# Kernel optimization log

Measured on AMD Instinct MI355X. Metric: run time of the kernel, lower is better.

Reference implementation:

```python
import jax, jax.numpy as jnp
import numpy as np

D_MODEL = 128
NUM_HEADS = 8
HEAD_DIM = D_MODEL // NUM_HEADS
LN_EPS = 1e-5


def layernorm(x, gamma, beta):
    mu = jnp.mean(x, axis=-1, keepdims=True)
    var = jnp.mean(jnp.square(x - mu), axis=-1, keepdims=True)
    return (x - mu) * jax.lax.rsqrt(var + LN_EPS) * gamma + beta


def setup_inputs() -> dict:
    key = jax.random.key(0)
    ks = jax.random.split(key, 12)
    B, L, d = 16, 1024, D_MODEL
    scale = 1.0 / np.sqrt(d)
    edge_x = jax.random.normal(ks[0], (B, L, d), dtype=jnp.float32)
    # True entries are masked out (masked_fill with -inf)
    edge_mask = jax.random.randint(ks[1], (B, L, L), 0, 2).astype(jnp.bool_)
    in_proj_w = jax.random.normal(ks[2], (d, 3 * d), dtype=jnp.float32) * scale  # fused QKV
    in_proj_b = jnp.zeros((3 * d,), dtype=jnp.float32)
    w1 = jax.random.normal(ks[3], (d, d), dtype=jnp.float32) * scale
    b1 = jnp.zeros((d,), dtype=jnp.float32)
    w2 = jax.random.normal(ks[4], (d, d), dtype=jnp.float32) * scale
    b2 = jnp.zeros((d,), dtype=jnp.float32)
    g1 = jnp.ones((d,), dtype=jnp.float32)
    beta1 = jnp.zeros((d,), dtype=jnp.float32)
    g2 = jnp.ones((d,), dtype=jnp.float32)
    beta2 = jnp.zeros((d,), dtype=jnp.float32)
    return {"edge_x": edge_x, "edge_mask": edge_mask, "in_proj_w": in_proj_w,
            "in_proj_b": in_proj_b, "w1": w1, "b1": b1, "w2": w2, "b2": b2,
            "g1": g1, "beta1": beta1, "g2": g2, "beta2": beta2}


def reference(edge_x, edge_mask, in_proj_w, in_proj_b, w1, b1, w2, b2, g1, beta1, g2, beta2):
    B, L, d = edge_x.shape
    H, hd = NUM_HEADS, HEAD_DIM
    scaling = float(hd) ** -0.5
    # fused QKV projection
    qkv = edge_x @ in_proj_w + in_proj_b              # [B, L, 3d]
    q, k, v = jnp.split(qkv, 3, axis=-1)
    q = q.reshape(B, L, H, hd).transpose(0, 2, 1, 3)  # [B, H, L, hd]
    k = k.reshape(B, L, H, hd).transpose(0, 2, 1, 3)
    v = v.reshape(B, L, H, hd).transpose(0, 2, 1, 3)
    scores = jnp.einsum('bhqd,bhkd->bhqk', q, k) * scaling  # [B, H, L, L]
    scores = jnp.where(edge_mask[:, None, :, :], -jnp.inf, scores)
    attn = jax.nn.softmax(scores, axis=-1)
    ctx = jnp.einsum('bhqk,bhkd->bhqd', attn, v)      # [B, H, L, hd]
    ctx = ctx.transpose(0, 2, 1, 3).reshape(B, L, d)
    # residual + LayerNorm
    x = layernorm(edge_x + ctx, g1, beta1)
    # FFN (relu), residual + LayerNorm (dropout=0 in eval mode)
    ff = jax.nn.relu(x @ w1 + b1) @ w2 + b2
    x = layernorm(x + ff, g2, beta2)
    return x
```

## Files before the change

kernel.cpp:

```cpp
#include <hip/hip_runtime.h>
#include <cstdint>

#define NROWS 16384
#define ARRE ((size_t)NROWS * 128)

typedef short short8 __attribute__((ext_vector_type(8)));
typedef float f32x4  __attribute__((ext_vector_type(4)));
typedef float f32x16 __attribute__((ext_vector_type(16)));

static __device__ __forceinline__ unsigned short f2bf(float f) {
    union { float f; uint32_t u; } v; v.f = f;
    uint32_t r = v.u + 0x7fffu + ((v.u >> 16) & 1u);
    return (unsigned short)(r >> 16);
}

static __device__ __forceinline__ uint32_t cvt_pk_bf16(float lo, float hi) {
    uint32_t r;
    asm("v_cvt_pk_bf16_f32 %0, %1, %2" : "=v"(r) : "v"(lo), "v"(hi));
    return r;
}

static __device__ __forceinline__ float v_exp2(float x) {
    float r;
    asm("v_exp_f32 %0, %1" : "=v"(r) : "v"(x));
    return r;
}

__global__ void k_castw(const float* __restrict__ wqkv, const float* __restrict__ w1,
                        const float* __restrict__ w2, unsigned short* __restrict__ wT,
                        const uint32_t* __restrict__ mask, int* __restrict__ flag)
{
    if (blockIdx.x == 320) {
        if (threadIdx.x == 0) {
            int f = 0;
            for (int i = 0; i < 256; ++i) f |= (mask[i] > 1u) ? 1 : 0;
            *flag = f;
        }
        return;
    }
    const int e = blockIdx.x * 256 + threadIdx.x;
    if (e < 49152) {
        const int n = e >> 7, k = e & 127;
        wT[e] = f2bf(wqkv[k * 384 + n]);
    } else if (e < 65536) {
        const int i = e - 49152, n = i >> 7, k = i & 127;
        wT[e] = f2bf(w1[k * 128 + n]);
    } else if (e < 81920) {
        const int i = e - 65536, n = i >> 7, k = i & 127;
        wT[e] = f2bf(w2[k * 128 + n]);
    }
}

template<int NF, int MODE>
__global__ __launch_bounds__(256, 2) void k_mm(const float* __restrict__ Xf,
        const unsigned short* __restrict__ Wt, const float* __restrict__ bias,
        unsigned short* __restrict__ out)
{
    __shared__ char smem[16384 + NF * 4096];
    char* const sX = smem;
    char* const sW = smem + 16384;
    const int t = threadIdx.x;
    const int w = t >> 6, l = t & 63;
    const int l4 = l >> 4, l15 = l & 15;
    const int r0 = blockIdx.x * 64;
    const int c0 = blockIdx.y * (NF * 16);

    #pragma unroll
    for (int i = 0; i < 4; ++i) {
        const int c = t + 256 * i;
        const int row = c >> 4, slot = c & 15;
        const float4* src = (const float4*)(Xf + (size_t)(r0 + row) * 128 + slot * 8);
        float4 f0 = src[0], f1 = src[1];
        uint4 v;
        v.x = cvt_pk_bf16(f0.x, f0.y);
        v.y = cvt_pk_bf16(f0.z, f0.w);
        v.z = cvt_pk_bf16(f1.x, f1.y);
        v.w = cvt_pk_bf16(f1.z, f1.w);
        *(uint4*)(sX + row * 256 + ((slot ^ (row & 15)) << 4)) = v;
    }
    #pragma unroll
    for (int i = 0; i < NF; ++i) {
        const int c = t + 256 * i;
        const int col = c >> 4, slot = c & 15;
        uint4 v = *(const uint4*)(Wt + (size_t)(c0 + col) * 128 + slot * 8);
        *(uint4*)(sW + col * 256 + ((slot ^ (col & 15)) << 4)) = v;
    }
    __syncthreads();

    short8 aF[4];
    #pragma unroll
    for (int kk = 0; kk < 4; ++kk)
        aF[kk] = *(const short8*)(sX + (w * 16 + l15) * 256 + (((kk * 4 + l4) ^ l15) << 4));

    f32x4 acc[NF];
    #pragma unroll
    for (int nf = 0; nf < NF; ++nf) acc[nf] = f32x4{0.f, 0.f, 0.f, 0.f};
    #pragma unroll
    for (int nf = 0; nf < NF; ++nf) {
        #pragma unroll
        for (int kk = 0; kk < 4; ++kk) {
            short8 bF = *(const short8*)(sW + (nf * 16 + l15) * 256 + (((kk * 4 + l4) ^ l15) << 4));
            acc[nf] = __builtin_amdgcn_mfma_f32_16x16x32_bf16(bF, aF[kk], acc[nf], 0, 0, 0);
        }
    }

    const float scl = (MODE == 0 && blockIdx.y == 0) ? 0.36067376022224085f : 1.0f;
    const int row = r0 + w * 16 + l15;
    #pragma unroll
    for (int nf = 0; nf < NF; ++nf) {
        const int cb = nf * 16 + l4 * 4;
        float4 bv = *(const float4*)(bias + c0 + cb);
        float v0 = acc[nf][0] + bv.x, v1 = acc[nf][1] + bv.y;
        float v2 = acc[nf][2] + bv.z, v3 = acc[nf][3] + bv.w;
        if (MODE == 1) {
            v0 = fmaxf(v0, 0.f); v1 = fmaxf(v1, 0.f);
            v2 = fmaxf(v2, 0.f); v3 = fmaxf(v3, 0.f);
        }
        v0 *= scl; v1 *= scl; v2 *= scl; v3 *= scl;
        uint2 pk;
        pk.x = cvt_pk_bf16(v0, v1);
        pk.y = cvt_pk_bf16(v2, v3);
        size_t o;
        if (MODE == 0) o = (size_t)blockIdx.y * ARRE + (size_t)row * 128 + cb;
        else           o = (size_t)row * 128 + c0 + cb;
        *(uint2*)(out + o) = pk;
    }
}

__global__ __launch_bounds__(256, 2) void k_ffn(const float* __restrict__ x1,
        const unsigned short* __restrict__ w1t, const float* __restrict__ b1,
        const unsigned short* __restrict__ w2t, const float* __restrict__ b2,
        const float* __restrict__ g2, const float* __restrict__ be2,
        float* __restrict__ out)
{
    __shared__ char smem[49152];
    char* const sX = smem;
    char* const sW = smem + 16384;
    const int t = threadIdx.x;
    const int w = t >> 6, l = t & 63;
    const int l4 = l >> 4, l15 = l & 15;
    const int r0 = blockIdx.x * 64;

    #pragma unroll
    for (int i = 0; i < 4; ++i) {
        const int c = t + 256 * i;
        const int row = c >> 4, slot = c & 15;
        const float4* src = (const float4*)(x1 + (size_t)(r0 + row) * 128 + slot * 8);
        float4 f0 = src[0], f1 = src[1];
        uint4 v;
        v.x = cvt_pk_bf16(f0.x, f0.y);
        v.y = cvt_pk_bf16(f0.z, f0.w);
        v.z = cvt_pk_bf16(f1.x, f1.y);
        v.w = cvt_pk_bf16(f1.z, f1.w);
        *(uint4*)(sX + row * 256 + ((slot ^ (row & 15)) << 4)) = v;
    }
    #pragma unroll
    for (int i = 0; i < 8; ++i) {
        const int c = t + 256 * i;
        const int col = c >> 4, slot = c & 15;
        uint4 v = *(const uint4*)(w1t + (size_t)col * 128 + slot * 8);
        *(uint4*)(sW + col * 256 + ((slot ^ (col & 15)) << 4)) = v;
    }
    __syncthreads();

    short8 aF[4];
    #pragma unroll
    for (int kk = 0; kk < 4; ++kk)
        aF[kk] = *(const short8*)(sX + (w * 16 + l15) * 256 + (((kk * 4 + l4) ^ l15) << 4));

    f32x4 acc[8];
    #pragma unroll
    for (int nf = 0; nf < 8; ++nf) acc[nf] = f32x4{0.f, 0.f, 0.f, 0.f};
    #pragma unroll
    for (int nf = 0; nf < 8; ++nf) {
        #pragma unroll
        for (int kk = 0; kk < 4; ++kk) {
            short8 bF = *(const short8*)(sW + (nf * 16 + l15) * 256 + (((kk * 4 + l4) ^ l15) << 4));
            acc[nf] = __builtin_amdgcn_mfma_f32_16x16x32_bf16(bF, aF[kk], acc[nf], 0, 0, 0);
        }
    }
    __syncthreads();

    {
        const int hrow = w * 16 + l15;
        #pragma unroll
        for (int nf = 0; nf < 8; ++nf) {
            const int cb = nf * 16 + l4 * 4;
            float4 bv = *(const float4*)(b1 + cb);
            float v0 = fmaxf(acc[nf][0] + bv.x, 0.f);
            float v1 = fmaxf(acc[nf][1] + bv.y, 0.f);
            float v2 = fmaxf(acc[nf][2] + bv.z, 0.f);
            float v3 = fmaxf(acc[nf][3] + bv.w, 0.f);
            uint2 pk;
            pk.x = cvt_pk_bf16(v0, v1);
            pk.y = cvt_pk_bf16(v2, v3);
            const int slot = (2 * nf) + (l4 >> 1);
            const int off  = (l4 & 1) * 8;
            *(uint2*)(sX + hrow * 256 + ((slot ^ (hrow & 15)) << 4) + off) = pk;
        }
    }
    #pragma unroll
    for (int i = 0; i < 8; ++i) {
        const int c = t + 256 * i;
        const int col = c >> 4, slot = c & 15;
        uint4 v = *(const uint4*)(w2t + (size_t)col * 128 + slot * 8);
        *(uint4*)(sW + col * 256 + ((slot ^ (col & 15)) << 4)) = v;
    }
    __syncthreads();

    short8 aG[4];
    #pragma unroll
    for (int kk = 0; kk < 4; ++kk)
        aG[kk] = *(const short8*)(sX + (w * 16 + l15) * 256 + (((kk * 4 + l4) ^ l15) << 4));

    f32x4 acc2[8];
    #pragma unroll
    for (int nf = 0; nf < 8; ++nf) acc2[nf] = f32x4{0.f, 0.f, 0.f, 0.f};
    #pragma unroll
    for (int nf = 0; nf < 8; ++nf) {
        #pragma unroll
        for (int kk = 0; kk < 4; ++kk) {
            short8 bF = *(const short8*)(sW + (nf * 16 + l15) * 256 + (((kk * 4 + l4) ^ l15) << 4));
            acc2[nf] = __builtin_amdgcn_mfma_f32_16x16x32_bf16(bF, aG[kk], acc2[nf], 0, 0, 0);
        }
    }

    const int row = r0 + w * 16 + l15;
    float y[8][4];
    float s = 0.f;
    #pragma unroll
    for (int nf = 0; nf < 8; ++nf) {
        const int cb = nf * 16 + l4 * 4;
        float4 bv = *(const float4*)(b2 + cb);
        float4 xv = *(const float4*)(x1 + (size_t)row * 128 + cb);
        y[nf][0] = acc2[nf][0] + bv.x + xv.x;
        y[nf][1] = acc2[nf][1] + bv.y + xv.y;
        y[nf][2] = acc2[nf][2] + bv.z + xv.z;
        y[nf][3] = acc2[nf][3] + bv.w + xv.w;
        s += y[nf][0] + y[nf][1] + y[nf][2] + y[nf][3];
    }
    s += __shfl_xor(s, 16); s += __shfl_xor(s, 32);
    const float mu = s * (1.f / 128.f);
    float vv = 0.f;
    #pragma unroll
    for (int nf = 0; nf < 8; ++nf) {
        #pragma unroll
        for (int reg = 0; reg < 4; ++reg) { float d = y[nf][reg] - mu; vv += d * d; }
    }
    vv += __shfl_xor(vv, 16); vv += __shfl_xor(vv, 32);
    const float rs = rsqrtf(vv * (1.f / 128.f) + 1e-5f);
    #pragma unroll
    for (int nf = 0; nf < 8; ++nf) {
        const int cb = nf * 16 + l4 * 4;
        float4 gv = *(const float4*)(g2 + cb);
        float4 ev = *(const float4*)(be2 + cb);
        float4 o;
        o.x = (y[nf][0] - mu) * rs * gv.x + ev.x;
        o.y = (y[nf][1] - mu) * rs * gv.y + ev.y;
        o.z = (y[nf][2] - mu) * rs * gv.z + ev.z;
        o.w = (y[nf][3] - mu) * rs * gv.w + ev.w;
        *(float4*)(out + (size_t)row * 128 + cb) = o;
    }
}

__global__ __launch_bounds__(512, 2) void k_attn(
        const unsigned short* __restrict__ qb,
        const unsigned short* __restrict__ kb,
        const unsigned short* __restrict__ vbp,
        const void* __restrict__ maskp, const int* __restrict__ flag,
        const float* __restrict__ x, const float* __restrict__ g1,
        const float* __restrict__ be1, float* __restrict__ x1)
{
    __shared__ alignas(16) char smem[41216];
    char*          const sK  = smem;
    char*          const sVT = smem + 9216;
    char*          const sP  = smem + 19584;
    unsigned char* const sM  = (unsigned char*)(smem + 40064);
    float*         const sS  = (float*)(smem + 40192);

    const int t  = threadIdx.x;
    const int w  = t >> 6;
    const int l  = t & 63;
    const int bid = blockIdx.x;
    const int b  = ((bid & 7) << 1) | ((bid >> 3) >> 5);
    const int q0 = ((bid >> 3) & 31) * 32;
    const int q   = l & 31;
    const int hi  = l >> 5;
    const int l4  = l >> 4;
    const int l15 = l & 15;
    const int bytemask = *flag;

    short8 qf;
    {
        const size_t qrow = (size_t)(b * 1024 + q0 + q) * 128;
        qf = *(const short8*)(qb + qrow + w * 16 + hi * 8);
    }
    float m = -INFINITY, ls = 0.f;
    f32x4 ac0 = {0,0,0,0}, ac1 = {0,0,0,0};
    const f32x16 z16 = {};
    float* const sSw = sS + w * 32;
    char*  const Pw  = sP + w * 2560;

    const uint8_t* m8  = (const uint8_t*)maskp;
    const int*     m32 = (const int*)maskp;

    for (int kt = 0; kt < 32; ++kt) {
        const int k0 = kt * 32;
        __syncthreads();
        {
            const int row = t >> 4, slot = t & 15;
            const size_t src = (size_t)(b * 1024 + k0 + row) * 128 + slot * 8;
            uint4 kv = *(const uint4*)(kb + src);
            *(uint4*)(sK + row * 288 + ((slot ^ (row & 15)) << 4)) = kv;
            uint4 vv = *(const uint4*)(vbp + src);
            char* vt = sVT + (slot >> 1) * 1296 + (slot & 1) * 640 + row * 2;
            const uint32_t w0 = vv.x, w1 = vv.y, w2 = vv.z, w3 = vv.w;
            *(unsigned short*)(vt + 0 * 80) = (unsigned short)(w0);
            *(unsigned short*)(vt + 1 * 80) = (unsigned short)(w0 >> 16);
            *(unsigned short*)(vt + 2 * 80) = (unsigned short)(w1);
            *(unsigned short*)(vt + 3 * 80) = (unsigned short)(w1 >> 16);
            *(unsigned short*)(vt + 4 * 80) = (unsigned short)(w2);
            *(unsigned short*)(vt + 5 * 80) = (unsigned short)(w2 >> 16);
            *(unsigned short*)(vt + 6 * 80) = (unsigned short)(w3);
            *(unsigned short*)(vt + 7 * 80) = (unsigned short)(w3 >> 16);
        }
        if (t < 128) {
            const int mq = t >> 2, g = t & 3;
            const size_t moff = ((size_t)b << 20) + (size_t)(q0 + mq) * 1024
                              + (size_t)(k0 + g * 8);
            unsigned int bits = 0;
            if (bytemask) {
                uint64_t v = *(const uint64_t*)(m8 + moff);
                #pragma unroll
                for (int j = 0; j < 8; ++j)
                    bits |= ((((v >> (8 * j)) & 0xffull) == 0ull) ? 1u : 0u) << j;
            } else {
                const int4* p = (const int4*)(m32 + moff);
                int4 va = p[0], vc = p[1];
                bits = (va.x==0?1u:0u) | (va.y==0?2u:0u) | (va.z==0?4u:0u) | (va.w==0?8u:0u)
                     | (vc.x==0?16u:0u) | (vc.y==0?32u:0u) | (vc.z==0?64u:0u) | (vc.w==0?128u:0u);
            }
            sM[mq * 4 + g] = (unsigned char)bits;
        }
        __syncthreads();

        const uint32_t mk = *(const uint32_t*)(sM + q * 4);
        const uint32_t mks = mk >> (4 * hi);

        short8 kf = *(const short8*)(sK + q * 288 + ((((w << 1) + hi) ^ (q & 15)) << 4));
        f32x16 sc = __builtin_amdgcn_mfma_f32_32x32x16_bf16(kf, qf, z16, 0, 0, 0);
        float sm = sc[0];
        #pragma unroll
        for (int r = 1; r < 16; ++r) sm = fmaxf(sm, sc[r]);
        sm = fmaxf(sm, __shfl_xor(sm, 32));
        if (__any(sm > m + 8.f)) {
            float nm = fmaxf(m, sm);
            float s  = v_exp2(m - nm);
            m = nm; ls *= s;
            sSw[q] = s;
            float4 s0v = *(float4*)&sSw[l4 * 4];
            float4 s1v = *(float4*)&sSw[l4 * 4 + 16];
            ac0[0] *= s0v.x; ac0[1] *= s0v.y; ac0[2] *= s0v.z; ac0[3] *= s0v.w;
            ac1[0] *= s1v.x; ac1[1] *= s1v.y; ac1[2] *= s1v.z; ac1[3] *= s1v.w;
        }
        float p[16]; float lsum = 0.f;
        #pragma unroll
        for (int r = 0; r < 16; ++r) {
            const int c = (r & 3) + 8 * (r >> 2);
            float pv = v_exp2(sc[r] - m);
            pv = ((mks >> c) & 1u) ? pv : 0.f;
            lsum += pv; p[r] = pv;
        }
        ls += lsum;
        #pragma unroll
        for (int g = 0; g < 4; ++g) {
            uint2 pk;
            pk.x = cvt_pk_bf16(p[4*g+0], p[4*g+1]);
            pk.y = cvt_pk_bf16(p[4*g+2], p[4*g+3]);
            *(uint2*)(Pw + q * 80 + (8 * g + 4 * hi) * 2) = pk;
        }
        short8 pa0 = *(const short8*)(Pw + l15 * 80 + l4 * 16);
        short8 pa1 = *(const short8*)(Pw + (l15 + 16) * 80 + l4 * 16);
        short8 vf  = *(const short8*)(sVT + w * 1296 + l15 * 80 + l4 * 16);
        ac0 = __builtin_amdgcn_mfma_f32_16x16x32_bf16(pa0, vf, ac0, 0, 0, 0);
        ac1 = __builtin_amdgcn_mfma_f32_16x16x32_bf16(pa1, vf, ac1, 0, 0, 0);
    }

    __syncthreads();
    float* const sC = (float*)smem;
    {
        float lt  = ls + __shfl_xor(ls, 32);
        float inv = 1.f / lt;
        sSw[q] = inv;
        float4 i0 = *(float4*)&sSw[l4 * 4];
        float4 i1 = *(float4*)&sSw[l4 * 4 + 16];
        const int cc = w * 16 + l15;
        sC[(l4 * 4 + 0) * 132 + cc]  = ac0[0] * i0.x;
        sC[(l4 * 4 + 1) * 132 + cc]  = ac0[1] * i0.y;
        sC[(l4 * 4 + 2) * 132 + cc]  = ac0[2] * i0.z;
        sC[(l4 * 4 + 3) * 132 + cc]  = ac0[3] * i0.w;
        sC[(l4 * 4 + 16) * 132 + cc] = ac1[0] * i1.x;
        sC[(l4 * 4 + 17) * 132 + cc] = ac1[1] * i1.y;
        sC[(l4 * 4 + 18) * 132 + cc] = ac1[2] * i1.z;
        sC[(l4 * 4 + 19) * 132 + cc] = ac1[3] * i1.w;
    }
    __syncthreads();

    {
        const int row = t >> 4;
        const int c0  = (t & 15) * 8;
        const size_t grow = (size_t)(b * 1024 + q0 + row);
        const float4* xp = (const float4*)(x + grow * 128 + c0);
        const float4* cp = (const float4*)(sC + row * 132 + c0);
        float y[8];
        float s = 0.f;
        #pragma unroll
        for (int j = 0; j < 2; ++j) {
            float4 xv = xp[j], cv = cp[j];
            y[4*j+0] = xv.x + cv.x; y[4*j+1] = xv.y + cv.y;
            y[4*j+2] = xv.z + cv.z; y[4*j+3] = xv.w + cv.w;
            s += y[4*j+0] + y[4*j+1] + y[4*j+2] + y[4*j+3];
        }
        s += __shfl_xor(s, 1); s += __shfl_xor(s, 2);
        s += __shfl_xor(s, 4); s += __shfl_xor(s, 8);
        const float mu = s * (1.f / 128.f);
        float vv = 0.f;
        #pragma unroll
        for (int e = 0; e < 8; ++e) { float d = y[e] - mu; vv += d * d; }
        vv += __shfl_xor(vv, 1); vv += __shfl_xor(vv, 2);
        vv += __shfl_xor(vv, 4); vv += __shfl_xor(vv, 8);
        const float rs = rsqrtf(vv * (1.f / 128.f) + 1e-5f);
        #pragma unroll
        for (int j = 0; j < 2; ++j) {
            float4 gv = *(const float4*)(g1 + c0 + 4 * j);
            float4 bv = *(const float4*)(be1 + c0 + 4 * j);
            float4 o;
            o.x = (y[4*j+0] - mu) * rs * gv.x + bv.x;
            o.y = (y[4*j+1] - mu) * rs * gv.y + bv.y;
            o.z = (y[4*j+2] - mu) * rs * gv.z + bv.z;
            o.w = (y[4*j+3] - mu) * rs * gv.w + bv.w;
            *(float4*)(x1 + grow * 128 + c0 + 4 * j) = o;
        }
    }
}

extern "C" void kernel_launch(void* const* d_in, const int* in_sizes, int n_in,
                              void* d_out, int out_size, void* d_ws, size_t ws_size,
                              hipStream_t stream)
{
    const float* x    = (const float*)d_in[0];
    const void*  mask = d_in[1];
    const float* wqkv = (const float*)d_in[2];
    const float* bqkv = (const float*)d_in[3];
    const float* w1   = (const float*)d_in[4];
    const float* b1   = (const float*)d_in[5];
    const float* w2   = (const float*)d_in[6];
    const float* b2   = (const float*)d_in[7];
    const float* g1   = (const float*)d_in[8];
    const float* be1  = (const float*)d_in[9];
    const float* g2   = (const float*)d_in[10];
    const float* be2  = (const float*)d_in[11];
    float* out = (float*)d_out;

    char* base = (char*)d_ws;
    int* flag = (int*)base;
    unsigned short* qb  = (unsigned short*)(base + 256);
    unsigned short* kb  = qb + ARRE;
    unsigned short* vb  = kb + ARRE;
    float* x1           = (float*)(base + 256 + (size_t)12 * 1024 * 1024);
    unsigned short* wT  = (unsigned short*)(base + 256 + (size_t)20 * 1024 * 1024);

    k_castw<<<321, 256, 0, stream>>>(wqkv, w1, w2, wT, (const uint32_t*)mask, flag);
    k_mm<8, 0><<<dim3(256, 3), 256, 0, stream>>>(x, wT, bqkv, qb);
    k_attn<<<512, 512, 0, stream>>>(qb, kb, vb, mask, flag, x, g1, be1, x1);
    k_ffn<<<256, 256, 0, stream>>>(x1, wT + 49152, b1, wT + 65536, b2, g2, be2, out);
}
```

Baseline: 197.5 us.

## Prefetch next K/V/mask tile into registers and keep P in registers for PV

The attention kernel now loads the next key tile's K, V and mask data into registers right after the barrier, so global loads overlap with compute instead of sitting in the critical path. The P·V product switches from two 16x16 MFMAs fed through an LDS staging buffer to two 32x32x16 MFMAs whose P operand is built with cross-half lane shuffles. This removes the sP and scale-broadcast LDS buffers and shrinks shared memory so launch bounds can request 4 blocks per CU. The trade-off is higher register pressure from the prefetch registers under a tighter register cap, and a redundant wraparound load on the last iteration.

```diff
diff --git a/kernel.cpp b/kernel.cpp
--- a/kernel.cpp
+++ b/kernel.cpp
@@ -263,7 +263,7 @@
     }
 }
 
-__global__ __launch_bounds__(512, 2) void k_attn(
+__global__ __launch_bounds__(512, 4) void k_attn(
         const unsigned short* __restrict__ qb,
         const unsigned short* __restrict__ kb,
         const unsigned short* __restrict__ vbp,
@@ -271,97 +271,112 @@
         const float* __restrict__ x, const float* __restrict__ g1,
         const float* __restrict__ be1, float* __restrict__ x1)
 {
-    __shared__ alignas(16) char smem[41216];
+    __shared__ alignas(16) char smem[18688];
     char*          const sK  = smem;
-    char*          const sVT = smem + 9216;
-    char*          const sP  = smem + 19584;
-    unsigned char* const sM  = (unsigned char*)(smem + 40064);
-    float*         const sS  = (float*)(smem + 40192);
+    char*          const sVT = smem + 8192;
+    unsigned char* const sM  = (unsigned char*)(smem + 18560);
 
     const int t  = threadIdx.x;
     const int w  = t >> 6;
     const int l  = t & 63;
     const int bid = blockIdx.x;
-    const int b  = ((bid & 7) << 1) | ((bid >> 3) >> 5);
+    const int b  = ((bid & 7) << 1) | (bid >> 8);
     const int q0 = ((bid >> 3) & 31) * 32;
-    const int q   = l & 31;
-    const int hi  = l >> 5;
-    const int l4  = l >> 4;
-    const int l15 = l & 15;
+    const int q  = l & 31;
+    const int hi = l >> 5;
     const int bytemask = *flag;
 
-    short8 qf;
-    {
-        const size_t qrow = (size_t)(b * 1024 + q0 + q) * 128;
-        qf = *(const short8*)(qb + qrow + w * 16 + hi * 8);
-    }
+    const short8 qf = *(const short8*)(qb + (size_t)(b * 1024 + q0 + q) * 128 + w * 16 + hi * 8);
+
+    const int srow = t >> 4, sslot = t & 15;
+    const size_t gbase = (size_t)(b * 1024 + srow) * 128 + sslot * 8;
+    char* const wK = sK + srow * 256 + ((sslot ^ (srow & 15)) << 4);
+    const int vh = sslot >> 1, vs = sslot & 1;
+    char* const wV = sVT + vh * 1296 + ((2 * srow + 16 * vs) & 63);
+    const int mq = t >> 2, mg = t & 3;
+    const size_t mbase = ((size_t)b << 20) + (size_t)(q0 + mq) * 1024 + mg * 8;
+
+    const char* const rK = sK + q * 256 + ((((w << 1) | hi) ^ (q & 15)) << 4);
+    const int dd = l & 15, sp = dd >> 3;
+    const char* const rV = sVT + w * 1296 + dd * 80;
+    const int vo0 = (16 * hi + 16 * sp) & 63;
+    const int vo1 = (32 + 16 * hi + 16 * sp) & 63;
+
+    uint4 kv, vv, ma = {0,0,0,0}, mb = {0,0,0,0};
+    kv = *(const uint4*)(kb + gbase);
+    vv = *(const uint4*)(vbp + gbase);
+    if (t < 128) {
+        if (bytemask) {
+            uint2 v = *(const uint2*)((const uint8_t*)maskp + mbase);
+            ma.x = v.x; ma.y = v.y;
+        } else {
+            const uint4* p4 = (const uint4*)((const int*)maskp + mbase);
+            ma = p4[0]; mb = p4[1];
+        }
+    }
+
     float m = -INFINITY, ls = 0.f;
-    f32x4 ac0 = {0,0,0,0}, ac1 = {0,0,0,0};
+    f32x16 acc = {};
     const f32x16 z16 = {};
-    float* const sSw = sS + w * 32;
-    char*  const Pw  = sP + w * 2560;
-
-    const uint8_t* m8  = (const uint8_t*)maskp;
-    const int*     m32 = (const int*)maskp;
+    union U8 { uint4 u; short8 s; };
 
     for (int kt = 0; kt < 32; ++kt) {
-        const int k0 = kt * 32;
         __syncthreads();
+        *(uint4*)wK = kv;
         {
-            const int row = t >> 4, slot = t & 15;
-            const size_t src = (size_t)(b * 1024 + k0 + row) * 128 + slot * 8;
-            uint4 kv = *(const uint4*)(kb + src);
-            *(uint4*)(sK + row * 288 + ((slot ^ (row & 15)) << 4)) = kv;
-            uint4 vv = *(const uint4*)(vbp + src);
-            char* vt = sVT + (slot >> 1) * 1296 + (slot & 1) * 640 + row * 2;
             const uint32_t w0 = vv.x, w1 = vv.y, w2 = vv.z, w3 = vv.w;
-            *(unsigned short*)(vt + 0 * 80) = (unsigned short)(w0);
-            *(unsigned short*)(vt + 1 * 80) = (unsigned short)(w0 >> 16);
-            *(unsigned short*)(vt + 2 * 80) = (unsigned short)(w1);
-            *(unsigned short*)(vt + 3 * 80) = (unsigned short)(w1 >> 16);
-            *(unsigned short*)(vt + 4 * 80) = (unsigned short)(w2);
-            *(unsigned short*)(vt + 5 * 80) = (unsigned short)(w2 >> 16);
-            *(unsigned short*)(vt + 6 * 80) = (unsigned short)(w3);
-            *(unsigned short*)(vt + 7 * 80) = (unsigned short)(w3 >> 16);
+            *(unsigned short*)(wV + (8 * vs + 0) * 80) = (unsigned short)(w0);
+            *(unsigned short*)(wV + (8 * vs + 1) * 80) = (unsigned short)(w0 >> 16);
+            *(unsigned short*)(wV + (8 * vs + 2) * 80) = (unsigned short)(w1);
+            *(unsigned short*)(wV + (8 * vs + 3) * 80) = (unsigned short)(w1 >> 16);
+            *(unsigned short*)(wV + (8 * vs + 4) * 80) = (unsigned short)(w2);
+            *(unsigned short*)(wV + (8 * vs + 5) * 80) = (unsigned short)(w2 >> 16);
+            *(unsigned short*)(wV + (8 * vs + 6) * 80) = (unsigned short)(w3);
+            *(unsigned short*)(wV + (8 * vs + 7) * 80) = (unsigned short)(w3 >> 16);
         }
         if (t < 128) {
-            const int mq = t >> 2, g = t & 3;
-            const size_t moff = ((size_t)b << 20) + (size_t)(q0 + mq) * 1024
-                              + (size_t)(k0 + g * 8);
             unsigned int bits = 0;
             if (bytemask) {
-                uint64_t v = *(const uint64_t*)(m8 + moff);
+                uint64_t v = (uint64_t)ma.x | ((uint64_t)ma.y << 32);
                 #pragma unroll
                 for (int j = 0; j < 8; ++j)
                     bits |= ((((v >> (8 * j)) & 0xffull) == 0ull) ? 1u : 0u) << j;
             } else {
-                const int4* p = (const int4*)(m32 + moff);
-                int4 va = p[0], vc = p[1];
-                bits = (va.x==0?1u:0u) | (va.y==0?2u:0u) | (va.z==0?4u:0u) | (va.w==0?8u:0u)
-                     | (vc.x==0?16u:0u) | (vc.y==0?32u:0u) | (vc.z==0?64u:0u) | (vc.w==0?128u:0u);
+                bits = (ma.x==0?1u:0u) | (ma.y==0?2u:0u) | (ma.z==0?4u:0u) | (ma.w==0?8u:0u)
+                     | (mb.x==0?16u:0u) | (mb.y==0?32u:0u) | (mb.z==0?64u:0u) | (mb.w==0?128u:0u);
             }
-            sM[mq * 4 + g] = (unsigned char)bits;
+            sM[mq * 4 + mg] = (unsigned char)bits;
         }
         __syncthreads();
-
-        const uint32_t mk = *(const uint32_t*)(sM + q * 4);
-        const uint32_t mks = mk >> (4 * hi);
-
-        short8 kf = *(const short8*)(sK + q * 288 + ((((w << 1) + hi) ^ (q & 15)) << 4));
+        {
+            const int kn = (kt + 1) & 31;
+            const size_t g = gbase + (size_t)kn * 4096;
+            kv = *(const uint4*)(kb + g);
+            vv = *(const uint4*)(vbp + g);
+            if (t < 128) {
+                const size_t mo = mbase + (size_t)kn * 32;
+                if (bytemask) {
+                    uint2 v = *(const uint2*)((const uint8_t*)maskp + mo);
+                    ma.x = v.x; ma.y = v.y;
+                } else {
+                    const uint4* p4 = (const uint4*)((const int*)maskp + mo);
+                    ma = p4[0]; mb = p4[1];
+                }
+            }
+        }
+        const uint32_t mks = (*(const uint32_t*)(sM + q * 4)) >> (4 * hi);
+        const short8 kf = *(const short8*)rK;
         f32x16 sc = __builtin_amdgcn_mfma_f32_32x32x16_bf16(kf, qf, z16, 0, 0, 0);
         float sm = sc[0];
         #pragma unroll
         for (int r = 1; r < 16; ++r) sm = fmaxf(sm, sc[r]);
         sm = fmaxf(sm, __shfl_xor(sm, 32));
         if (__any(sm > m + 8.f)) {
-            float nm = fmaxf(m, sm);
-            float s  = v_exp2(m - nm);
+            const float nm = fmaxf(m, sm);
+            const float s = v_exp2(m - nm);
             m = nm; ls *= s;
-            sSw[q] = s;
-            float4 s0v = *(float4*)&sSw[l4 * 4];
-            float4 s1v = *(float4*)&sSw[l4 * 4 + 16];
-            ac0[0] *= s0v.x; ac0[1] *= s0v.y; ac0[2] *= s0v.z; ac0[3] *= s0v.w;
-            ac1[0] *= s1v.x; ac1[1] *= s1v.y; ac1[2] *= s1v.z; ac1[3] *= s1v.w;
+            #pragma unroll
+            for (int r = 0; r < 8; ++r) acc[r] *= s;
         }
         float p[16]; float lsum = 0.f;
         #pragma unroll
@@ -372,37 +387,32 @@
             lsum += pv; p[r] = pv;
         }
         ls += lsum;
-        #pragma unroll
-        for (int g = 0; g < 4; ++g) {
-            uint2 pk;
-            pk.x = cvt_pk_bf16(p[4*g+0], p[4*g+1]);
-            pk.y = cvt_pk_bf16(p[4*g+2], p[4*g+3]);
-            *(uint2*)(Pw + q * 80 + (8 * g + 4 * hi) * 2) = pk;
-        }
-        short8 pa0 = *(const short8*)(Pw + l15 * 80 + l4 * 16);
-        short8 pa1 = *(const short8*)(Pw + (l15 + 16) * 80 + l4 * 16);
-        short8 vf  = *(const short8*)(sVT + w * 1296 + l15 * 80 + l4 * 16);
-        ac0 = __builtin_amdgcn_mfma_f32_16x16x32_bf16(pa0, vf, ac0, 0, 0, 0);
-        ac1 = __builtin_amdgcn_mfma_f32_16x16x32_bf16(pa1, vf, ac1, 0, 0, 0);
+        const uint32_t cA0 = cvt_pk_bf16(p[0],  p[1]),  cA1 = cvt_pk_bf16(p[2],  p[3]);
+        const uint32_t cB0 = cvt_pk_bf16(p[4],  p[5]),  cB1 = cvt_pk_bf16(p[6],  p[7]);
+        const uint32_t cC0 = cvt_pk_bf16(p[8],  p[9]),  cC1 = cvt_pk_bf16(p[10], p[11]);
+        const uint32_t cD0 = cvt_pk_bf16(p[12], p[13]), cD1 = cvt_pk_bf16(p[14], p[15]);
+        const uint32_t xA0 = __shfl_xor(cA0, 32), xA1 = __shfl_xor(cA1, 32);
+        const uint32_t xB0 = __shfl_xor(cB0, 32), xB1 = __shfl_xor(cB1, 32);
+        const uint32_t xC0 = __shfl_xor(cC0, 32), xC1 = __shfl_xor(cC1, 32);
+        const uint32_t xD0 = __shfl_xor(cD0, 32), xD1 = __shfl_xor(cD1, 32);
+        U8 pb0, pb1;
+        pb0.u = hi ? uint4{xB0, xB1, cB0, cB1} : uint4{cA0, cA1, xA0, xA1};
+        pb1.u = hi ? uint4{xD0, xD1, cD0, cD1} : uint4{cC0, cC1, xC0, xC1};
+        const short8 va0 = *(const short8*)(rV + vo0);
+        const short8 va1 = *(const short8*)(rV + vo1);
+        acc = __builtin_amdgcn_mfma_f32_32x32x16_bf16(va0, pb0.s, acc, 0, 0, 0);
+        acc = __builtin_amdgcn_mfma_f32_32x32x16_bf16(va1, pb1.s, acc, 0, 0, 0);
     }
 
     __syncthreads();
     float* const sC = (float*)smem;
     {
-        float lt  = ls + __shfl_xor(ls, 32);
-        float inv = 1.f / lt;
-        sSw[q] = inv;
-        float4 i0 = *(float4*)&sSw[l4 * 4];
-        float4 i1 = *(float4*)&sSw[l4 * 4 + 16];
-        const int cc = w * 16 + l15;
-        sC[(l4 * 4 + 0) * 132 + cc]  = ac0[0] * i0.x;
-        sC[(l4 * 4 + 1) * 132 + cc]  = ac0[1] * i0.y;
-        sC[(l4 * 4 + 2) * 132 + cc]  = ac0[2] * i0.z;
-        sC[(l4 * 4 + 3) * 132 + cc]  = ac0[3] * i0.w;
-        sC[(l4 * 4 + 16) * 132 + cc] = ac1[0] * i1.x;
-        sC[(l4 * 4 + 17) * 132 + cc] = ac1[1] * i1.y;
-        sC[(l4 * 4 + 18) * 132 + cc] = ac1[2] * i1.z;
-        sC[(l4 * 4 + 19) * 132 + cc] = ac1[3] * i1.w;
+        const float inv = 1.f / (ls + __shfl_xor(ls, 32));
+        float* const row = sC + q * 132 + w * 16 + 4 * hi;
+        row[0] = acc[0] * inv; row[1] = acc[1] * inv;
+        row[2] = acc[2] * inv; row[3] = acc[3] * inv;
+        row[8] = acc[4] * inv; row[9] = acc[5] * inv;
+        row[10] = acc[6] * inv; row[11] = acc[7] * inv;
     }
     __syncthreads();
 
@@ -424,12 +434,12 @@
         s += __shfl_xor(s, 1); s += __shfl_xor(s, 2);
         s += __shfl_xor(s, 4); s += __shfl_xor(s, 8);
         const float mu = s * (1.f / 128.f);
-        float vv = 0.f;
-        #pragma unroll
-        for (int e = 0; e < 8; ++e) { float d = y[e] - mu; vv += d * d; }
-        vv += __shfl_xor(vv, 1); vv += __shfl_xor(vv, 2);
-        vv += __shfl_xor(vv, 4); vv += __shfl_xor(vv, 8);
-        const float rs = rsqrtf(vv * (1.f / 128.f) + 1e-5f);
+        float vv2 = 0.f;
+        #pragma unroll
+        for (int e = 0; e < 8; ++e) { float d = y[e] - mu; vv2 += d * d; }
+        vv2 += __shfl_xor(vv2, 1); vv2 += __shfl_xor(vv2, 2);
+        vv2 += __shfl_xor(vv2, 4); vv2 += __shfl_xor(vv2, 8);
+        const float rs = rsqrtf(vv2 * (1.f / 128.f) + 1e-5f);
         #pragma unroll
         for (int j = 0; j < 2; ++j) {
             float4 gv = *(const float4*)(g1 + c0 + 4 * j);
```

Measured after the change: 184.9 us. 6.4% less time.
